# Kernel optimization log

Hardware: AMD Instinct MI355X
Metric: run time of the kernel (lower is better)

Reference implementation:

```python
import jax, jax.numpy as jnp
import numpy as np
import math

EMBED_DIM = 1024
NUM_HEADS = 16
HEAD_DIM = EMBED_DIM // NUM_HEADS
ROPE_BASE = 10000.0


def setup_inputs() -> dict:
    key = jax.random.key(0)
    ks = jax.random.split(key, 11)
    B, S, E = 2, 2048, EMBED_DIM
    s = 1.0 / math.sqrt(E)
    return {
        "query": jax.random.normal(ks[0], (B, S, E), jnp.float32),
        "key": jax.random.normal(ks[1], (B, S, E), jnp.float32),
        "value": jax.random.normal(ks[2], (B, S, E), jnp.float32),
        "Wq": jax.random.normal(ks[3], (E, E), jnp.float32) * s,
        "bq": jnp.zeros((E,), jnp.float32),
        "Wk": jax.random.normal(ks[4], (E, E), jnp.float32) * s,
        "bk": jnp.zeros((E,), jnp.float32),
        "Wv": jax.random.normal(ks[5], (E, E), jnp.float32) * s,
        "bv": jnp.zeros((E,), jnp.float32),
        "Wo": jax.random.normal(ks[6], (E, E), jnp.float32) * s,
        "bo": jnp.zeros((E,), jnp.float32),
    }


def _rope_cache(S, D, dtype):
    inv_freq = 1.0 / (ROPE_BASE ** (jnp.arange(0, D, 2, dtype=jnp.float32) / D))
    t = jnp.arange(S, dtype=jnp.float32)
    freqs = t[:, None] * inv_freq[None, :]  # [S, D/2]
    return jnp.cos(freqs).astype(dtype), jnp.sin(freqs).astype(dtype)


def _apply_rope(x, cos, sin):
    # x: [B, H, S, D]; cos/sin: [S, D/2]
    x_even = x[..., 0::2]
    x_odd = x[..., 1::2]
    rot_even = x_even * cos - x_odd * sin
    rot_odd = x_odd * cos + x_even * sin
    # interleave back: [..., D/2, 2] -> [..., D]
    return jnp.stack([rot_even, rot_odd], axis=-1).reshape(x.shape)


def reference(query, key, value, Wq, bq, Wk, bk, Wv, bv, Wo, bo):
    B, S, E = query.shape
    H, D = NUM_HEADS, HEAD_DIM
    q = (query @ Wq.T + bq).reshape(B, S, H, D).transpose(0, 2, 1, 3)
    k = (key @ Wk.T + bk).reshape(B, S, H, D).transpose(0, 2, 1, 3)
    v = (value @ Wv.T + bv).reshape(B, S, H, D).transpose(0, 2, 1, 3)
    cos, sin = _rope_cache(S, D, q.dtype)
    q = _apply_rope(q, cos, sin)
    k = _apply_rope(k, cos, sin)
    scores = jnp.einsum('bhsd,bhtd->bhst', q, k) / math.sqrt(D)
    attn = jax.nn.softmax(scores, axis=-1)
    out = jnp.einsum('bhst,bhtd->bhsd', attn, v)
    out = out.transpose(0, 2, 1, 3).reshape(B, S, E)
    return out @ Wo.T + bo
```

## Files before the change

### kernel.cpp

```cpp
#include <hip/hip_runtime.h>
#include <math.h>

typedef unsigned short u16;
typedef __bf16 bf16x8 __attribute__((ext_vector_type(8)));
typedef float floatx4 __attribute__((ext_vector_type(4)));
typedef float floatx16 __attribute__((ext_vector_type(16)));

#define MFMA16(a, b, c) __builtin_amdgcn_mfma_f32_16x16x32_bf16((a), (b), (c), 0, 0, 0)
#define MFMA32(a, b, c) __builtin_amdgcn_mfma_f32_32x32x16_bf16((a), (b), (c), 0, 0, 0)

__device__ __forceinline__ float bf2f(u16 u) {
  union { float f; unsigned int i; } v; v.i = ((unsigned int)u) << 16; return v.f;
}
__device__ __forceinline__ u16 f2bf(float f) {
  __bf16 h = (__bf16)f;
  union { __bf16 h; u16 u; } v; v.h = h; return v.u;
}
__device__ __forceinline__ bf16x8 cvt8(float4 a, float4 b) {
  bf16x8 r;
  r[0] = (__bf16)a.x; r[1] = (__bf16)a.y; r[2] = (__bf16)a.z; r[3] = (__bf16)a.w;
  r[4] = (__bf16)b.x; r[5] = (__bf16)b.y; r[6] = (__bf16)b.z; r[7] = (__bf16)b.w;
  return r;
}
__device__ __forceinline__ void gl2lds16(const void* g, void* l) {
  __builtin_amdgcn_global_load_lds(
      (const __attribute__((address_space(1))) unsigned int*)g,
      (__attribute__((address_space(3))) unsigned int*)l, 16, 0, 0);
}

struct CvtArgs { const float* src[4]; u16* dst[4]; };
__global__ __launch_bounds__(256) void cvt_kernel(CvtArgs a) {
  const float* s = a.src[blockIdx.z];
  u16* d = a.dst[blockIdx.z];
  const int i = (blockIdx.x * 256 + threadIdx.x) * 8;
  const float4 x = *reinterpret_cast<const float4*>(s + i);
  const float4 y = *reinterpret_cast<const float4*>(s + i + 4);
  *reinterpret_cast<bf16x8*>(&d[i]) = cvt8(x, y);
}

struct GemmArgs {
  const void* A[3];
  const void* W[3];
  const float* bias[3];
  void* C[3];
  int out_mode[3];
};

template <int BM, int ABF16, int WBF16>
__global__ __launch_bounds__(256) void gemm_nt(GemmArgs args) {
  const int N = 1024, K = 1024;

  const int NY = gridDim.y;
  const int lin = blockIdx.x + (blockIdx.y << 3) + blockIdx.z * (NY << 3);
  const int chunk = NY * gridDim.z;
  const int nid = (lin & 7) * chunk + (lin >> 3);
  const int z = nid / (NY << 3);
  const int rem = nid - z * (NY << 3);
  const int m0 = (rem >> 3) * BM, n0 = (rem & 7) * 128;

  const float* bias = args.bias[z];
  const int out_mode = args.out_mode[z];
  constexpr int MI = BM / 32;

  __shared__ __align__(16) char AsB[ABF16 ? BM * 64 : BM * 128];
  __shared__ __align__(16) char BsB[WBF16 ? 128 * 64 : 128 * 128];

  const int t = threadIdx.x;
  const int wave = t >> 6, lane = t & 63;
  const int lr = lane & 15, quad = lane >> 4;
  const int wm = (wave >> 1) * (BM / 2), wn = (wave & 1) * 64;

  auto stage = [&](int kt) {
    if constexpr (ABF16) {
      const u16* Ab = (const u16*)args.A[z];
      constexpr int NI = BM / 16;
#pragma unroll
      for (int j = 0; j < (NI + 3) / 4; j++) {
        const int ii = wave + j * 4;
        if (NI >= 4 || ii < NI) {
          const int r0 = ii * 16;
          const int row = r0 + (lane >> 2);
          const int cg = (lane & 3) ^ ((lane >> 2) & 3);
          gl2lds16(Ab + (size_t)(m0 + row) * K + kt + cg * 8, AsB + r0 * 64 + lane * 16);
        }
      }
    } else {
      const float* Af = (const float*)args.A[z];
#pragma unroll
      for (int j = 0; j < BM / 32; j++) {
        const int r0 = wave * (BM / 4) + j * 8;
        const int row = r0 + (lane >> 3);
        const int cg = (lane & 7) ^ ((lane >> 3) & 7);
        gl2lds16(Af + (size_t)(m0 + row) * K + kt + cg * 4, AsB + r0 * 128 + lane * 16);
      }
    }
    if constexpr (WBF16) {
      const u16* Wb = (const u16*)args.W[z];
#pragma unroll
      for (int j = 0; j < 2; j++) {
        const int r0 = (wave + j * 4) * 16;
        const int row = r0 + (lane >> 2);
        const int cg = (lane & 3) ^ ((lane >> 2) & 3);
        gl2lds16(Wb + (size_t)(n0 + row) * K + kt + cg * 8, BsB + r0 * 64 + lane * 16);
      }
    } else {
      const float* Wf = (const float*)args.W[z];
#pragma unroll
      for (int j = 0; j < 4; j++) {
        const int r0 = wave * 32 + j * 8;
        const int row = r0 + (lane >> 3);
        const int cg = (lane & 7) ^ ((lane >> 3) & 7);
        gl2lds16(Wf + (size_t)(n0 + row) * K + kt + cg * 4, BsB + r0 * 128 + lane * 16);
      }
    }
  };

  floatx4 acc[MI][4] = {};

  for (int kt = 0; kt < K; kt += 32) {
    __syncthreads();
    stage(kt);
    __syncthreads();

    bf16x8 af[MI], bf[4];
#pragma unroll
    for (int i = 0; i < MI; i++) {
      const int row = wm + i * 16 + lr;
      if constexpr (ABF16) {
        const int cp = quad ^ (row & 3);
        af[i] = *reinterpret_cast<const bf16x8*>(AsB + row * 64 + cp * 16);
      } else {
        const int e = row & 7;
        const float4 c0 = *reinterpret_cast<const float4*>(AsB + row * 128 + ((2 * quad) ^ e) * 16);
        const float4 c1 = *reinterpret_cast<const float4*>(AsB + row * 128 + ((2 * quad + 1) ^ e) * 16);
        af[i] = cvt8(c0, c1);
      }
    }
#pragma unroll
    for (int i = 0; i < 4; i++) {
      const int row = wn + i * 16 + lr;
      if constexpr (WBF16) {
        const int cp = quad ^ (row & 3);
        bf[i] = *reinterpret_cast<const bf16x8*>(BsB + row * 64 + cp * 16);
      } else {
        const int e = row & 7;
        const float4 c0 = *reinterpret_cast<const float4*>(BsB + row * 128 + ((2 * quad) ^ e) * 16);
        const float4 c1 = *reinterpret_cast<const float4*>(BsB + row * 128 + ((2 * quad + 1) ^ e) * 16);
        bf[i] = cvt8(c0, c1);
      }
    }
#pragma unroll
    for (int mi = 0; mi < MI; mi++)
#pragma unroll
      for (int nf = 0; nf < 4; nf++)
        acc[mi][nf] = MFMA16(af[mi], bf[nf], acc[mi][nf]);
  }

#pragma unroll
  for (int nf = 0; nf < 4; nf++) {
    const int col = n0 + wn + nf * 16 + lr;
    const float bv = bias[col];
#pragma unroll
    for (int mi = 0; mi < MI; mi++) {
      const int row0 = m0 + wm + mi * 16 + quad * 4;
      if (out_mode == 0) {
        u16* C = (u16*)args.C[z];
#pragma unroll
        for (int r = 0; r < 4; r++)
          C[(row0 + r) * N + col] = f2bf(acc[mi][nf][r] + bv);
      } else if (out_mode == 1) {
        u16* C = (u16*)args.C[z];
        const int h = col >> 6, d = col & 63;
        const int b = row0 >> 11, s = row0 & 2047;
        ushort4 pk;
        pk.x = f2bf(acc[mi][nf][0] + bv);
        pk.y = f2bf(acc[mi][nf][1] + bv);
        pk.z = f2bf(acc[mi][nf][2] + bv);
        pk.w = f2bf(acc[mi][nf][3] + bv);
        *reinterpret_cast<ushort4*>(&C[((b * 16 + h) * 64 + d) * 2048 + s]) = pk;
      } else {
        float* C = (float*)args.C[z];
#pragma unroll
        for (int r = 0; r < 4; r++)
          C[(row0 + r) * N + col] = acc[mi][nf][r] + bv;
      }
    }
  }
}

__global__ __launch_bounds__(256) void rope_kernel(u16* Kb) {
  const int idx = blockIdx.x * 256 + threadIdx.x;
  const int row = idx >> 7;
  const int cg = idx & 127;
  const int s = row & 2047;
  const int col0 = cg * 8;
  union { uint4 u; u16 h[8]; } v;
  v.u = *reinterpret_cast<const uint4*>(&Kb[row * 1024 + col0]);
  const int j0 = (col0 & 63) >> 1;
#pragma unroll
  for (int p = 0; p < 4; p++) {
    const int j = j0 + p;
    const float inv = exp2f(-(float)j * (13.287712379549449f / 32.0f));
    const float f = (float)s * inv;
    float sn, cs;
    sincosf(f, &sn, &cs);
    const float e = bf2f(v.h[2 * p]), o = bf2f(v.h[2 * p + 1]);
    v.h[2 * p]     = f2bf(e * cs - o * sn);
    v.h[2 * p + 1] = f2bf(o * cs + e * sn);
  }
  *reinterpret_cast<uint4*>(&Kb[row * 1024 + col0]) = v.u;
}

#define MAKE_PB(pp, g, out) do {                                              \
    unsigned int wA, wB, wC, wD;                                              \
    asm("v_cvt_pk_bf16_f32 %0, %1, %2" : "=v"(wA) : "v"((pp)[(g)+0]), "v"((pp)[(g)+1])); \
    asm("v_cvt_pk_bf16_f32 %0, %1, %2" : "=v"(wB) : "v"((pp)[(g)+4]), "v"((pp)[(g)+5])); \
    asm("v_cvt_pk_bf16_f32 %0, %1, %2" : "=v"(wC) : "v"((pp)[(g)+2]), "v"((pp)[(g)+3])); \
    asm("v_cvt_pk_bf16_f32 %0, %1, %2" : "=v"(wD) : "v"((pp)[(g)+6]), "v"((pp)[(g)+7])); \
    asm("v_permlane32_swap_b32 %0, %1" : "+v"(wA), "+v"(wB));                 \
    asm("v_permlane32_swap_b32 %0, %1" : "+v"(wC), "+v"(wD));                 \
    union { unsigned int w[4]; bf16x8 v; } u_;                                \
    u_.w[0] = wA; u_.w[1] = wC; u_.w[2] = wB; u_.w[3] = wD;                   \
    (out) = u_.v;                                                             \
  } while (0)

__global__ __launch_bounds__(256, 2) void attn_kernel(const u16* Q, const u16* K,
                                                      const u16* Vt, u16* O) {
  const int lin = blockIdx.x + (blockIdx.y << 4);
  const int nid = (lin & 7) * 64 + (lin >> 3);
  const int bx = nid & 15, bh = nid >> 4;

  const int b = bh >> 4, h = bh & 15;
  const int t = threadIdx.x;
  const int warp = t >> 6, lane = t & 63;
  const int lq = lane & 31, hi = lane >> 5;

  __shared__ __align__(16) u16 Ks[2][64][64];
  __shared__ __align__(16) u16 Vs[2][64][64];

  const int q0 = bx * 128 + warp * 32;

  const u16* qp = &Q[(size_t)(b * 2048 + q0 + lq) * 1024 + h * 64 + hi * 8];
  bf16x8 qf[4];
#pragma unroll
  for (int s = 0; s < 4; s++) qf[s] = *reinterpret_cast<const bf16x8*>(&qp[s * 16]);

  {
    const float seqf = (float)(q0 + lq);
#pragma unroll
    for (int s = 0; s < 4; s++) {
#pragma unroll
      for (int p = 0; p < 4; p++) {
        const int jp = s * 8 + hi * 4 + p;
        const float inv = exp2f(-(float)jp * (13.287712379549449f / 32.0f));
        float sn, cs;
        sincosf(seqf * inv, &sn, &cs);
        const float e = (float)qf[s][2 * p], o = (float)qf[s][2 * p + 1];
        qf[s][2 * p]     = (__bf16)((e * cs - o * sn) * 0.18033688011112042f);
        qf[s][2 * p + 1] = (__bf16)((o * cs + e * sn) * 0.18033688011112042f);
      }
    }
  }

  const u16* kbase = &K[(size_t)b * 2048 * 1024 + h * 64];
  const u16* vbase = &Vt[(size_t)bh * 131072];

  const int srr = lane >> 3;
  const int scg = (lane & 7) ^ srr;

  auto stage = [&](int kt2, int bufi) {
#pragma unroll
    for (int j = 0; j < 2; j++) {
      const int r0 = warp * 16 + j * 8;
      const int row = r0 + srr;
      gl2lds16(kbase + (size_t)(kt2 + row) * 1024 + scg * 8, &Ks[bufi][r0][0]);
      gl2lds16(vbase + (size_t)row * 2048 + kt2 + scg * 8, &Vs[bufi][r0][0]);
    }
  };

  floatx16 o0 = {}, o1 = {};
  float m = -1.0e30f, l = 0.0f;

  stage(0, 0);
  int buf = 0;
  for (int kt = 0; kt < 2048; kt += 64) {
    __syncthreads();
    if (kt + 64 < 2048) stage(kt + 64, buf ^ 1);

    bf16x8 kf[2][4], vf[4][2];
#pragma unroll
    for (int kb = 0; kb < 2; kb++) {
      const int r = kb * 32 + lq;
#pragma unroll
      for (int s = 0; s < 4; s++)
        kf[kb][s] = *reinterpret_cast<const bf16x8*>(&Ks[buf][r][((s * 2 + hi) ^ (r & 7)) * 8]);
    }
#pragma unroll
    for (int d = 0; d < 2; d++) {
      const int r = d * 32 + lq;
#pragma unroll
      for (int ks = 0; ks < 4; ks++)
        vf[ks][d] = *reinterpret_cast<const bf16x8*>(&Vs[buf][r][((ks * 2 + hi) ^ (r & 7)) * 8]);
    }

    floatx16 p0 = {}, p1 = {};
#pragma unroll
    for (int s = 0; s < 4; s++) {
      p0 = MFMA32(kf[0][s], qf[s], p0);
      p1 = MFMA32(kf[1][s], qf[s], p1);
    }

    float mx = p0[0];
#pragma unroll
    for (int r = 1; r < 16; r++) mx = fmaxf(mx, p0[r]);
#pragma unroll
    for (int r = 0; r < 16; r++) mx = fmaxf(mx, p1[r]);
    mx = fmaxf(mx, __shfl_xor(mx, 32, 64));
    if (!__all(mx <= m + 10.0f)) {
      const float mn = fmaxf(m, mx);
      const float al = __builtin_amdgcn_exp2f(m - mn);
      m = mn;
      l *= al;
#pragma unroll
      for (int r = 0; r < 16; r++) { o0[r] *= al; o1[r] *= al; }
    }
    float sum = 0.0f;
#pragma unroll
    for (int r = 0; r < 16; r++) { p0[r] = __builtin_amdgcn_exp2f(p0[r] - m); sum += p0[r]; }
#pragma unroll
    for (int r = 0; r < 16; r++) { p1[r] = __builtin_amdgcn_exp2f(p1[r] - m); sum += p1[r]; }
    l += sum + __shfl_xor(sum, 32, 64);

    bf16x8 pb0, pb1, pb2, pb3;
    MAKE_PB(p0, 0, pb0);
    MAKE_PB(p0, 8, pb1);
    MAKE_PB(p1, 0, pb2);
    MAKE_PB(p1, 8, pb3);

    o0 = MFMA32(vf[0][0], pb0, o0);
    o1 = MFMA32(vf[0][1], pb0, o1);
    o0 = MFMA32(vf[1][0], pb1, o0);
    o1 = MFMA32(vf[1][1], pb1, o1);
    o0 = MFMA32(vf[2][0], pb2, o0);
    o1 = MFMA32(vf[2][1], pb2, o1);
    o0 = MFMA32(vf[3][0], pb3, o0);
    o1 = MFMA32(vf[3][1], pb3, o1);

    buf ^= 1;
  }

  const float rl = 1.0f / l;
  u16* op = &O[(size_t)(b * 2048 + q0 + lq) * 1024 + h * 64 + hi * 4];
#pragma unroll
  for (int rq = 0; rq < 4; rq++) {
    ushort4 s0, s1;
    s0.x = f2bf(o0[4 * rq + 0] * rl); s0.y = f2bf(o0[4 * rq + 1] * rl);
    s0.z = f2bf(o0[4 * rq + 2] * rl); s0.w = f2bf(o0[4 * rq + 3] * rl);
    s1.x = f2bf(o1[4 * rq + 0] * rl); s1.y = f2bf(o1[4 * rq + 1] * rl);
    s1.z = f2bf(o1[4 * rq + 2] * rl); s1.w = f2bf(o1[4 * rq + 3] * rl);
    *reinterpret_cast<ushort4*>(&op[rq * 8]) = s0;
    *reinterpret_cast<ushort4*>(&op[rq * 8 + 32]) = s1;
  }
}

extern "C" void kernel_launch(void* const* d_in, const int* in_sizes, int n_in,
                              void* d_out, int out_size, void* d_ws, size_t ws_size,
                              hipStream_t stream) {
  (void)in_sizes; (void)n_in; (void)out_size;
  const float* query = (const float*)d_in[0];
  const float* key   = (const float*)d_in[1];
  const float* value = (const float*)d_in[2];
  const float* Wq = (const float*)d_in[3];
  const float* bq = (const float*)d_in[4];
  const float* Wk = (const float*)d_in[5];
  const float* bk = (const float*)d_in[6];
  const float* Wv = (const float*)d_in[7];
  const float* bv = (const float*)d_in[8];
  const float* Wo = (const float*)d_in[9];
  const float* bo = (const float*)d_in[10];

  u16* Qb = (u16*)d_ws;
  u16* Kb = (u16*)d_out;
  u16* Vt = (u16*)d_out + 4194304;

  const bool haveW = ws_size >= (size_t)(8388608 + 4 * 2097152);
  const bool haveA = ws_size >= (size_t)(8388608 + 4 * 2097152 + 25165824);
  u16* Wbf = (u16*)d_ws + 4194304;
  u16* Abf = (u16*)d_ws + 4194304 + 4194304;

  if (haveW) {
    CvtArgs cw;
    cw.src[0] = Wq; cw.dst[0] = Wbf;
    cw.src[1] = Wk; cw.dst[1] = Wbf + 1048576;
    cw.src[2] = Wv; cw.dst[2] = Wbf + 2097152;
    cw.src[3] = Wo; cw.dst[3] = Wbf + 3145728;
    cvt_kernel<<<dim3(512, 1, 4), dim3(256), 0, stream>>>(cw);
  }
  if (haveA) {
    CvtArgs ca;
    ca.src[0] = query; ca.dst[0] = Abf;
    ca.src[1] = key;   ca.dst[1] = Abf + 4194304;
    ca.src[2] = value; ca.dst[2] = Abf + 8388608;
    ca.src[3] = query; ca.dst[3] = Abf;
    cvt_kernel<<<dim3(2048, 1, 3), dim3(256), 0, stream>>>(ca);
  }

  GemmArgs g1;
  g1.bias[0] = bq; g1.C[0] = Qb; g1.out_mode[0] = 0;
  g1.bias[1] = bk; g1.C[1] = Kb; g1.out_mode[1] = 0;
  g1.bias[2] = bv; g1.C[2] = Vt; g1.out_mode[2] = 1;
  if (haveA) {
    g1.A[0] = Abf; g1.A[1] = Abf + 4194304; g1.A[2] = Abf + 8388608;
  } else {
    g1.A[0] = query; g1.A[1] = key; g1.A[2] = value;
  }
  if (haveW) {
    g1.W[0] = Wbf; g1.W[1] = Wbf + 1048576; g1.W[2] = Wbf + 2097152;
  } else {
    g1.W[0] = Wq; g1.W[1] = Wk; g1.W[2] = Wv;
  }
  if (haveA && haveW)
    gemm_nt<128, 1, 1><<<dim3(8, 32, 3), dim3(256), 0, stream>>>(g1);
  else if (haveW)
    gemm_nt<128, 0, 1><<<dim3(8, 32, 3), dim3(256), 0, stream>>>(g1);
  else
    gemm_nt<128, 0, 0><<<dim3(8, 32, 3), dim3(256), 0, stream>>>(g1);

  rope_kernel<<<dim3(2048), dim3(256), 0, stream>>>(Kb);

  attn_kernel<<<dim3(16, 32), dim3(256), 0, stream>>>(Qb, Kb, Vt, Qb);

  GemmArgs g2;
  for (int i = 0; i < 3; i++) {
    g2.A[i] = Qb; g2.bias[i] = bo;
    g2.C[i] = d_out; g2.out_mode[i] = 2;
    g2.W[i] = haveW ? (const void*)(Wbf + 3145728) : (const void*)Wo;
  }
  if (haveW)
    gemm_nt<64, 1, 1><<<dim3(8, 64, 1), dim3(256), 0, stream>>>(g2);
  else
    gemm_nt<64, 1, 0><<<dim3(8, 64, 1), dim3(256), 0, stream>>>(g2);
}
```

Measured before the change: 224.4 us.

## Split KV range across warp pairs in attention and merge partial softmax

```diff
diff --git a/kernel.cpp b/kernel.cpp
--- a/kernel.cpp
+++ b/kernel.cpp
@@ -224,8 +224,8 @@
     (out) = u_.v;                                                             \
   } while (0)
 
-__global__ __launch_bounds__(256, 2) void attn_kernel(const u16* Q, const u16* K,
-                                                      const u16* Vt, u16* O) {
+__global__ __launch_bounds__(512) void attn_kernel(const u16* Q, const u16* K,
+                                                   const u16* Vt, u16* O) {
   const int lin = blockIdx.x + (blockIdx.y << 4);
   const int nid = (lin & 7) * 64 + (lin >> 3);
   const int bx = nid & 15, bh = nid >> 4;
@@ -234,11 +234,14 @@
   const int t = threadIdx.x;
   const int warp = t >> 6, lane = t & 63;
   const int lq = lane & 31, hi = lane >> 5;
-
-  __shared__ __align__(16) u16 Ks[2][64][64];
-  __shared__ __align__(16) u16 Vs[2][64][64];
-
-  const int q0 = bx * 128 + warp * 32;
+  const int pair = warp >> 1, w = warp & 1;
+
+  __shared__ __align__(16) u16 Ks[2][2][64][64];
+  __shared__ __align__(16) u16 Vs[2][2][64][64];
+  __shared__ float Mlm[4][2][32], Mll[4][2][32];
+
+  const int q0 = bx * 128 + pair * 32;
+  const int k0 = w * 1024;
 
   const u16* qp = &Q[(size_t)(b * 2048 + q0 + lq) * 1024 + h * 64 + hi * 8];
   bf16x8 qf[4];
@@ -271,36 +274,31 @@
   auto stage = [&](int kt2, int bufi) {
 #pragma unroll
     for (int j = 0; j < 2; j++) {
-      const int r0 = warp * 16 + j * 8;
+      const int r0 = pair * 16 + j * 8;
       const int row = r0 + srr;
-      gl2lds16(kbase + (size_t)(kt2 + row) * 1024 + scg * 8, &Ks[bufi][r0][0]);
-      gl2lds16(vbase + (size_t)row * 2048 + kt2 + scg * 8, &Vs[bufi][r0][0]);
+      gl2lds16(kbase + (size_t)(kt2 + row) * 1024 + scg * 8, &Ks[w][bufi][r0][0]);
+      gl2lds16(vbase + (size_t)row * 2048 + kt2 + scg * 8, &Vs[w][bufi][r0][0]);
     }
   };
 
   floatx16 o0 = {}, o1 = {};
   float m = -1.0e30f, l = 0.0f;
 
-  stage(0, 0);
-  int buf = 0;
-  for (int kt = 0; kt < 2048; kt += 64) {
-    __syncthreads();
-    if (kt + 64 < 2048) stage(kt + 64, buf ^ 1);
-
+  auto compute = [&](int buf) {
     bf16x8 kf[2][4], vf[4][2];
 #pragma unroll
     for (int kb = 0; kb < 2; kb++) {
       const int r = kb * 32 + lq;
 #pragma unroll
       for (int s = 0; s < 4; s++)
-        kf[kb][s] = *reinterpret_cast<const bf16x8*>(&Ks[buf][r][((s * 2 + hi) ^ (r & 7)) * 8]);
+        kf[kb][s] = *reinterpret_cast<const bf16x8*>(&Ks[w][buf][r][((s * 2 + hi) ^ (r & 7)) * 8]);
     }
 #pragma unroll
     for (int d = 0; d < 2; d++) {
       const int r = d * 32 + lq;
 #pragma unroll
       for (int ks = 0; ks < 4; ks++)
-        vf[ks][d] = *reinterpret_cast<const bf16x8*>(&Vs[buf][r][((ks * 2 + hi) ^ (r & 7)) * 8]);
+        vf[ks][d] = *reinterpret_cast<const bf16x8*>(&Vs[w][buf][r][((ks * 2 + hi) ^ (r & 7)) * 8]);
     }
 
     floatx16 p0 = {}, p1 = {};
@@ -345,21 +343,51 @@
     o1 = MFMA32(vf[2][1], pb2, o1);
     o0 = MFMA32(vf[3][0], pb3, o0);
     o1 = MFMA32(vf[3][1], pb3, o1);
-
+  };
+
+  stage(k0, 0);
+  int buf = 0;
+  for (int i = 0; i < 16; i++) {
+    __syncthreads();
+    if (i + 1 < 16) stage(k0 + (i + 1) * 64, buf ^ 1);
+    compute(buf);
     buf ^= 1;
   }
 
-  const float rl = 1.0f / l;
-  u16* op = &O[(size_t)(b * 2048 + q0 + lq) * 1024 + h * 64 + hi * 4];
-#pragma unroll
-  for (int rq = 0; rq < 4; rq++) {
-    ushort4 s0, s1;
-    s0.x = f2bf(o0[4 * rq + 0] * rl); s0.y = f2bf(o0[4 * rq + 1] * rl);
-    s0.z = f2bf(o0[4 * rq + 2] * rl); s0.w = f2bf(o0[4 * rq + 3] * rl);
-    s1.x = f2bf(o1[4 * rq + 0] * rl); s1.y = f2bf(o1[4 * rq + 1] * rl);
-    s1.z = f2bf(o1[4 * rq + 2] * rl); s1.w = f2bf(o1[4 * rq + 3] * rl);
-    *reinterpret_cast<ushort4*>(&op[rq * 8]) = s0;
-    *reinterpret_cast<ushort4*>(&op[rq * 8 + 32]) = s1;
+  float (*Ox)[32][64] = reinterpret_cast<float (*)[32][64]>(&Ks[0][0][0][0]);
+  if (hi == 0) { Mlm[pair][w][lq] = m; Mll[pair][w][lq] = l; }
+  __syncthreads();
+  const float mo = Mlm[pair][w ^ 1][lq];
+  const float lo = Mll[pair][w ^ 1][lq];
+  const float ms = fmaxf(m, mo);
+  const float f  = __builtin_amdgcn_exp2f(m - ms);
+  const float fo = __builtin_amdgcn_exp2f(mo - ms);
+  const float ltot = l * f + lo * fo;
+  if (w == 1) {
+#pragma unroll
+    for (int r = 0; r < 16; r++) {
+      Ox[pair][r][lane] = o0[r] * f;
+      Ox[pair][16 + r][lane] = o1[r] * f;
+    }
+  }
+  __syncthreads();
+  if (w == 0) {
+    const float rl = 1.0f / ltot;
+    u16* op = &O[(size_t)(b * 2048 + q0 + lq) * 1024 + h * 64 + hi * 4];
+#pragma unroll
+    for (int rq = 0; rq < 4; rq++) {
+      ushort4 s0, s1;
+      s0.x = f2bf((o0[4 * rq + 0] * f + Ox[pair][4 * rq + 0][lane]) * rl);
+      s0.y = f2bf((o0[4 * rq + 1] * f + Ox[pair][4 * rq + 1][lane]) * rl);
+      s0.z = f2bf((o0[4 * rq + 2] * f + Ox[pair][4 * rq + 2][lane]) * rl);
+      s0.w = f2bf((o0[4 * rq + 3] * f + Ox[pair][4 * rq + 3][lane]) * rl);
+      s1.x = f2bf((o1[4 * rq + 0] * f + Ox[pair][16 + 4 * rq + 0][lane]) * rl);
+      s1.y = f2bf((o1[4 * rq + 1] * f + Ox[pair][16 + 4 * rq + 1][lane]) * rl);
+      s1.z = f2bf((o1[4 * rq + 2] * f + Ox[pair][16 + 4 * rq + 2][lane]) * rl);
+      s1.w = f2bf((o1[4 * rq + 3] * f + Ox[pair][16 + 4 * rq + 3][lane]) * rl);
+      *reinterpret_cast<ushort4*>(&op[rq * 8]) = s0;
+      *reinterpret_cast<ushort4*>(&op[rq * 8 + 32]) = s1;
+    }
   }
 }
 
@@ -428,7 +456,7 @@
 
   rope_kernel<<<dim3(2048), dim3(256), 0, stream>>>(Kb);
 
-  attn_kernel<<<dim3(16, 32), dim3(256), 0, stream>>>(Qb, Kb, Vt, Qb);
+  attn_kernel<<<dim3(16, 32), dim3(512), 0, stream>>>(Qb, Kb, Vt, Qb);
 
   GemmArgs g2;
   for (int i = 0; i < 3; i++) {
```

After: 245.4 us. 1.09x slower.
